# Performance work log

Hardware: AMD Instinct MI355X
Metric: run time of the kernel (lower is better)

The kernel has to match this reference:

```python
import jax, jax.numpy as jnp
import numpy as np

D = 1024   # hidden_size
H = 16     # n_head
K = 64     # head_size
B = 4
T = 1024
LAYER_ID = 12
NUM_LAYERS = 24
D_MIX = 32
D_DECAY = 64


def setup_inputs() -> dict:
    key = jax.random.key(0)
    ks = jax.random.split(key, 12)
    r01 = LAYER_ID / (NUM_LAYERS - 1)          # ratio_0_to_1
    r10 = 1.0 - LAYER_ID / NUM_LAYERS          # ratio_1_to_almost0
    ddd = jnp.arange(D, dtype=jnp.float32) / D
    maa = lambda p: (1.0 - ddd ** p).reshape(1, 1, D)
    inp = {}
    inp['x'] = jax.random.normal(ks[0], (B, T, D), jnp.float32)
    inp['time_maa_x'] = maa(r10)
    inp['time_maa_w'] = maa(r10)
    inp['time_maa_k'] = maa(r10)
    inp['time_maa_v'] = (1.0 - (ddd ** r10 + 0.3 * r01)).reshape(1, 1, D)
    inp['time_maa_r'] = maa(0.5 * r10)
    inp['time_maa_g'] = maa(0.5 * r10)
    # torch inits time_maa_w1 to zeros (trivial); use small uniform like w2 for a non-degenerate test
    inp['time_maa_w1'] = jax.random.uniform(ks[1], (D, D_MIX * 5), jnp.float32, -0.01, 0.01)
    inp['time_maa_w2'] = jax.random.uniform(ks[2], (5, D_MIX, D), jnp.float32, -0.01, 0.01)
    n = jnp.arange(D, dtype=jnp.float32)
    inp['time_decay'] = (-6.0 + 5.0 * (n / (D - 1)) ** (0.7 + 1.3 * r01)).reshape(1, 1, D)
    inp['time_decay_w1'] = jax.random.uniform(ks[3], (D, D_DECAY), jnp.float32, -0.01, 0.01)
    inp['time_decay_w2'] = jax.random.uniform(ks[4], (D_DECAY, D), jnp.float32, -0.01, 0.01)
    for nm, kk in zip(['W_r', 'W_k', 'W_v', 'W_g', 'W_o'], ks[5:10]):
        inp[nm] = jax.random.normal(kk, (D, D), jnp.float32) * 0.02
    inp['ln_w'] = jnp.ones((D,), jnp.float32)
    inp['ln_b'] = jnp.zeros((D,), jnp.float32)
    return inp


def _bidir_shift(x):
    # (x[i-1] + x[i+1]) / 2 with zero padding at the boundaries
    left = jnp.pad(x[:, :-1, :], ((0, 0), (1, 0), (0, 0)))
    right = jnp.pad(x[:, 1:, :], ((0, 0), (0, 1), (0, 0)))
    return 0.5 * (left + right)


def _lion_attention(r, k, v, w):
    # r,k,v,w: (B,H,T,Khd), w = -exp(decay) <= 0
    Tn = r.shape[2]
    cs = jnp.cumsum(w, axis=2)
    cs_b = cs - w
    shift_f = cs[:, :, Tn // 2:Tn // 2 + 1, :]
    shift_b = cs_b[:, :, Tn // 2:Tn // 2 + 1, :]
    cf = jnp.clip(cs - shift_f, -60.0, 60.0)
    cb = jnp.clip(cs_b - shift_b, -60.0, 60.0)
    # A_fwd = tril(Q*e^{cf} @ (K*e^{-cf})^T); A_bwd = triu(Q*e^{-cb} @ (K*e^{cb})^T, 1)
    A_f = jnp.einsum('bhik,bhjk->bhij', r * jnp.exp(cf), k * jnp.exp(-cf))
    A_b = jnp.einsum('bhik,bhjk->bhij', r * jnp.exp(-cb), k * jnp.exp(cb))
    idx = jnp.arange(Tn)
    lower = idx[:, None] >= idx[None, :]   # tril incl. diagonal
    A = jnp.where(lower, A_f, A_b)         # == tril(A_f) + triu(A_b, 1)
    return jnp.einsum('bhij,bhjk->bhik', A, v)


def reference(x, time_maa_x, time_maa_w, time_maa_k, time_maa_v, time_maa_r, time_maa_g,
              time_maa_w1, time_maa_w2, time_decay, time_decay_w1, time_decay_w2,
              W_r, W_k, W_v, W_g, W_o, ln_w, ln_b):
    Bn, Tn, Dn = x.shape
    Hh, Kk = H, Dn // H
    dxprev = _bidir_shift(x) - x
    # data-dependent token-shift mixing coefficients (LoRA-style)
    xxx = jnp.tanh((x + dxprev * time_maa_x) @ time_maa_w1)          # (B,T,5*32)
    mm = jnp.einsum('btfm,fmd->fbtd', xxx.reshape(Bn, Tn, 5, D_MIX), time_maa_w2)
    mw, mk, mv, mr, mg = mm[0], mm[1], mm[2], mm[3], mm[4]
    xw = x + dxprev * (time_maa_w + mw)
    xk = x + dxprev * (time_maa_k + mk)
    xv = x + dxprev * (time_maa_v + mv)
    xr = x + dxprev * (time_maa_r + mr)
    xg = x + dxprev * (time_maa_g + mg)
    r = xr @ W_r.T
    k = xk @ W_k.T
    v = xv @ W_v.T
    g = jax.nn.silu(xg @ W_g.T)
    w = time_decay + jnp.tanh(xw @ time_decay_w1) @ time_decay_w2   # (B,T,D)
    to_h = lambda t: t.reshape(Bn, Tn, Hh, Kk).transpose(0, 2, 1, 3)
    y = _lion_attention(to_h(r), to_h(k), to_h(v), -jnp.exp(to_h(w)))
    y = y.transpose(0, 2, 1, 3).reshape(Bn * Tn, Dn)
    # GroupNorm(n_head groups, eps = 1e-5 * head_size_divisor^2)
    eps = 1e-5 * 64.0
    yg = y.reshape(Bn * Tn, Hh, Kk)
    mu = jnp.mean(yg, axis=-1, keepdims=True)
    var = jnp.var(yg, axis=-1, keepdims=True)
    yn = ((yg - mu) * jax.lax.rsqrt(var + eps)).reshape(Bn * Tn, Dn) * ln_w + ln_b
    y = yn.reshape(Bn, Tn, Dn)
    return (y * g) @ W_o.T
```

## Files before the change

kernel.cpp:

```cpp
#include <hip/hip_runtime.h>
#include <math.h>

#define NB 4
#define TT 1024
#define DD 1024
#define NTOK 4096
#define ND (NTOK*DD)

typedef __attribute__((ext_vector_type(8))) short bh8;
typedef __attribute__((ext_vector_type(4))) float fx4;

__device__ __forceinline__ unsigned short f2bf(float f) {
    unsigned int b = __float_as_uint(f);
    b += 0x7fffu + ((b >> 16) & 1u);
    return (unsigned short)(b >> 16);
}

__device__ __forceinline__ unsigned pkbf(float a, float b) {
#if __has_builtin(__builtin_amdgcn_cvt_pk_bf16_f32)
    auto r = __builtin_amdgcn_cvt_pk_bf16_f32(a, b);
    unsigned u;
    __builtin_memcpy(&u, &r, 4);
    return u;
#else
    return ((unsigned)f2bf(b) << 16) | f2bf(a);
#endif
}

#define GLD16(gp, lp) __builtin_amdgcn_global_load_lds( \
    (__attribute__((address_space(1))) void*)(gp), \
    (__attribute__((address_space(3))) void*)(lp), 16, 0, 0)

#define BARF() do { __builtin_amdgcn_s_barrier(); asm volatile("" ::: "memory"); } while (0)

__global__ __launch_bounds__(256) void k_prep(const float* __restrict__ W_r, const float* __restrict__ W_k,
                                              const float* __restrict__ W_v, const float* __restrict__ W_g,
                                              const float* __restrict__ W_o,
                                              const float* __restrict__ w1, const float* __restrict__ dw1,
                                              const float* __restrict__ w2,
                                              unsigned short* __restrict__ Wrb, unsigned short* __restrict__ Wkb,
                                              unsigned short* __restrict__ Wvb, unsigned short* __restrict__ Wgb,
                                              unsigned short* __restrict__ Wob,
                                              unsigned short* __restrict__ w1T, unsigned short* __restrict__ dw1T,
                                              unsigned short* __restrict__ w2T16) {
    int y = blockIdx.y, bx = blockIdx.x, tid = threadIdx.x;
    if (y < 5) {
        if (bx >= 512) return;
        const float* s = (y == 0) ? W_r : (y == 1) ? W_k : (y == 2) ? W_v : (y == 3) ? W_g : W_o;
        unsigned short* d = (y == 0) ? Wrb : (y == 1) ? Wkb : (y == 2) ? Wvb : (y == 3) ? Wgb : Wob;
        int i = (bx * 256 + tid) * 8;
        float4 a = *(const float4*)(s + i);
        float4 b = *(const float4*)(s + i + 4);
        uint4 o;
        o.x = pkbf(a.x, a.y);
        o.y = pkbf(a.z, a.w);
        o.z = pkbf(b.x, b.y);
        o.w = pkbf(b.z, b.w);
        *(uint4*)(d + i) = o;
    } else if (y == 5) {
        int o = bx * 256 + tid;
        int r = o & 1023, c = o >> 10;
        w1T[o] = f2bf(w1[r * 160 + c]);
    } else {
        if (bx < 256) {
            int o = bx * 256 + tid;
            int r = o & 1023, c = o >> 10;
            dw1T[o] = f2bf(dw1[r * 64 + c]);
        } else if (bx < 276) {
            int wi = bx - 256;
            int f = wi >> 2;
            int d = (wi & 3) * 256 + tid;
#pragma unroll 8
            for (int m = 0; m < 32; m++)
                w2T16[(size_t)(f * 1024 + d) * 32 + m] = f2bf(w2[(size_t)(f * 32 + m) * 1024 + d]);
        }
    }
}

__global__ __launch_bounds__(256) void k_mixx(const float* __restrict__ x,
                                              const float* __restrict__ maa_x,
                                              unsigned short* __restrict__ xmix16) {
    int base = (blockIdx.x * 256 + threadIdx.x) * 4;
    int t = (base >> 10) & 1023;
    int d = base & 1023;
    float4 xv = *(const float4*)(x + base);
    float4 xm = (t > 0)    ? *(const float4*)(x + base - 1024) : make_float4(0, 0, 0, 0);
    float4 xp = (t < 1023) ? *(const float4*)(x + base + 1024) : make_float4(0, 0, 0, 0);
    float4 ma = *(const float4*)(maa_x + d);
    uint2 o;
    float a0 = xv.x + (0.5f * (xm.x + xp.x) - xv.x) * ma.x;
    float a1 = xv.y + (0.5f * (xm.y + xp.y) - xv.y) * ma.y;
    float a2 = xv.z + (0.5f * (xm.z + xp.z) - xv.z) * ma.z;
    float a3 = xv.w + (0.5f * (xm.w + xp.w) - xv.w) * ma.w;
    o.x = pkbf(a0, a1);
    o.y = pkbf(a2, a3);
    *(uint2*)(xmix16 + base) = o;
}

__global__ __launch_bounds__(64) void k_xxx2(const unsigned short* __restrict__ xmix16,
                                             const unsigned short* __restrict__ w1T,
                                             unsigned short* __restrict__ xxx16) {
    int lane = threadIdx.x;
    int l15 = lane & 15, qd = lane >> 4;
    int m0 = blockIdx.x * 16;
    fx4 acc[10];
#pragma unroll
    for (int nt = 0; nt < 10; nt++)
#pragma unroll
        for (int r = 0; r < 4; r++) acc[nt][r] = 0.f;
#pragma unroll 2
    for (int kb = 0; kb < 1024; kb += 32) {
        bh8 af = *(const bh8*)(xmix16 + (size_t)(m0 + l15) * 1024 + kb + qd * 8);
#pragma unroll
        for (int nt = 0; nt < 10; nt++) {
            bh8 bf = *(const bh8*)(w1T + (size_t)(nt * 16 + l15) * 1024 + kb + qd * 8);
            acc[nt] = __builtin_amdgcn_mfma_f32_16x16x32_bf16(af, bf, acc[nt], 0, 0, 0);
        }
    }
#pragma unroll
    for (int nt = 0; nt < 10; nt++)
#pragma unroll
        for (int r = 0; r < 4; r++)
            xxx16[(size_t)(m0 + qd * 4 + r) * 160 + nt * 16 + l15] = f2bf(tanhf(acc[nt][r]));
}

__global__ __launch_bounds__(256, 2) void k_mmix(const float* __restrict__ x,
                                                 const unsigned short* __restrict__ xxx16,
                                                 const unsigned short* __restrict__ w2T16,
                                                 const float* __restrict__ maa_w,
                                                 const float* __restrict__ maa_k,
                                                 const float* __restrict__ maa_v,
                                                 const float* __restrict__ maa_r,
                                                 const float* __restrict__ maa_g,
                                                 unsigned short* __restrict__ xw16,
                                                 unsigned short* __restrict__ xk16,
                                                 unsigned short* __restrict__ xv16,
                                                 unsigned short* __restrict__ xr16,
                                                 unsigned short* __restrict__ xg16) {
    int tid = threadIdx.x;
    int w = tid >> 6, lane = tid & 63, l15 = lane & 15, qd = lane >> 4;
    int n0 = blockIdx.x * 64;
    int m0w = blockIdx.y * 128 + w * 32;
    const float* maap[5] = {maa_w, maa_k, maa_v, maa_r, maa_g};
    unsigned short* outp[5] = {xw16, xk16, xv16, xr16, xg16};
    float xin[8][4], dxv[8][4];
#pragma unroll
    for (int mi = 0; mi < 2; mi++)
#pragma unroll
        for (int r = 0; r < 4; r++) {
            int tok = m0w + mi * 16 + qd * 4 + r;
            int t = tok & 1023;
#pragma unroll
            for (int ni = 0; ni < 4; ni++) {
                int d = n0 + ni * 16 + l15;
                size_t idx = (size_t)tok * 1024 + d;
                float xv = x[idx];
                float xm1 = (t > 0)    ? x[idx - 1024] : 0.f;
                float xp1 = (t < 1023) ? x[idx + 1024] : 0.f;
                xin[mi * 4 + r][ni] = xv;
                dxv[mi * 4 + r][ni] = 0.5f * (xm1 + xp1) - xv;
            }
        }
#pragma unroll
    for (int f = 0; f < 5; f++) {
        bh8 af[2], bf[4];
#pragma unroll
        for (int mi = 0; mi < 2; mi++)
            af[mi] = *(const bh8*)(xxx16 + (size_t)(m0w + mi * 16 + l15) * 160 + f * 32 + qd * 8);
#pragma unroll
        for (int ni = 0; ni < 4; ni++)
            bf[ni] = *(const bh8*)(w2T16 + (size_t)(f * 1024 + n0 + ni * 16 + l15) * 32 + qd * 8);
        fx4 acc[2][4];
#pragma unroll
        for (int mi = 0; mi < 2; mi++)
#pragma unroll
            for (int ni = 0; ni < 4; ni++) {
#pragma unroll
                for (int r = 0; r < 4; r++) acc[mi][ni][r] = 0.f;
                acc[mi][ni] = __builtin_amdgcn_mfma_f32_16x16x32_bf16(af[mi], bf[ni], acc[mi][ni], 0, 0, 0);
            }
        const float* maa = maap[f];
        unsigned short* op = outp[f];
#pragma unroll
        for (int ni = 0; ni < 4; ni++) {
            float mv = maa[n0 + ni * 16 + l15];
#pragma unroll
            for (int mi = 0; mi < 2; mi++)
#pragma unroll
                for (int r = 0; r < 4; r++) {
                    float o = xin[mi * 4 + r][ni] + dxv[mi * 4 + r][ni] * (mv + acc[mi][ni][r]);
                    op[(size_t)(m0w + mi * 16 + qd * 4 + r) * 1024 + n0 + ni * 16 + l15] = f2bf(o);
                }
        }
    }
}

__global__ __launch_bounds__(64) void k_dec1m(const unsigned short* __restrict__ xw16,
                                              const unsigned short* __restrict__ dw1T,
                                              float* __restrict__ dech) {
    int lane = threadIdx.x;
    int l15 = lane & 15, qd = lane >> 4;
    int m0 = blockIdx.x * 16;
    fx4 acc[4];
#pragma unroll
    for (int nt = 0; nt < 4; nt++)
#pragma unroll
        for (int r = 0; r < 4; r++) acc[nt][r] = 0.f;
#pragma unroll 2
    for (int kb = 0; kb < 1024; kb += 32) {
        bh8 af = *(const bh8*)(xw16 + (size_t)(m0 + l15) * 1024 + kb + qd * 8);
#pragma unroll
        for (int nt = 0; nt < 4; nt++) {
            bh8 bf = *(const bh8*)(dw1T + (size_t)(nt * 16 + l15) * 1024 + kb + qd * 8);
            acc[nt] = __builtin_amdgcn_mfma_f32_16x16x32_bf16(af, bf, acc[nt], 0, 0, 0);
        }
    }
#pragma unroll
    for (int nt = 0; nt < 4; nt++)
#pragma unroll
        for (int r = 0; r < 4; r++)
            dech[(size_t)(m0 + qd * 4 + r) * 64 + nt * 16 + l15] = tanhf(acc[nt][r]);
}

__global__ __launch_bounds__(256) void k_dec2(const float* __restrict__ dech,
                                              const float* __restrict__ dw2,
                                              const float* __restrict__ tdec,
                                              float* __restrict__ ew) {
    __shared__ float hl[8][64];
    int tid = threadIdx.x;
    int tok0 = blockIdx.x * 8;
    {
        int l = tid;        hl[l >> 6][l & 63] = dech[tok0 * 64 + l];
        l = tid + 256;      hl[l >> 6][l & 63] = dech[tok0 * 64 + l];
    }
    __syncthreads();
#pragma unroll 1
    for (int c = 0; c < 4; c++) {
        int d = c * 256 + tid;
        float acc[8] = {};
#pragma unroll 8
        for (int j = 0; j < 64; j++) {
            float wv = dw2[j * 1024 + d];
#pragma unroll
            for (int g = 0; g < 8; g++) acc[g] = fmaf(hl[g][j], wv, acc[g]);
        }
        float td = tdec[d];
#pragma unroll
        for (int g = 0; g < 8; g++) ew[(tok0 + g) * 1024 + d] = -expf(td + acc[g]);
    }
}

__global__ __launch_bounds__(64) void k_scan1(const float* __restrict__ ew, float* __restrict__ segsum) {
    int bx = blockIdx.x;
    int b = bx >> 9, seg = (bx >> 4) & 31, dch = bx & 15;
    int d = dch * 64 + threadIdx.x;
    size_t base = ((size_t)(b * 1024 + seg * 32)) * 1024 + d;
    float s = 0.f;
#pragma unroll 8
    for (int t = 0; t < 32; t++) s += ew[base + (size_t)t * 1024];
    segsum[(b * 32 + seg) * 1024 + d] = s;
}

__global__ __launch_bounds__(64) void k_scan3(const float* __restrict__ ew, const float* __restrict__ segsum,
                                              float* __restrict__ cf, float* __restrict__ cb) {
    int bx = blockIdx.x;
    int b = bx >> 9, seg = (bx >> 4) & 31, dch = bx & 15;
    int d = dch * 64 + threadIdx.x;
    float run = 0.f, pre = 0.f, off16 = 0.f;
#pragma unroll
    for (int s = 0; s < 32; s++) {
        float tv = segsum[(b * 32 + s) * 1024 + d];
        if (s == seg) pre = run;
        if (s == 16) off16 = run;
        run += tv;
    }
    float e512 = ew[((size_t)(b * 1024 + 512)) * 1024 + d];
    float sb = off16;
    float sf = off16 + e512;
    float cum = pre;
    size_t base = ((size_t)(b * 1024 + seg * 32)) * 1024 + d;
#pragma unroll 4
    for (int t = 0; t < 32; t++) {
        float prev = cum;
        cum += ew[base + (size_t)t * 1024];
        cf[base + (size_t)t * 1024] = fminf(fmaxf(cum - sf, -60.f), 60.f);
        cb[base + (size_t)t * 1024] = fminf(fmaxf(prev - sb, -60.f), 60.f);
    }
}

#define QST(slotoff, kbv) do { \
    unsigned short* _sa = (unsigned short*)(smem + (slotoff)); \
    unsigned short* _sb = _sa + 8192; \
    GLD16(aSrc + (size_t)(kbv),             _sa + (w * 64) * 32); \
    GLD16(aSrc + (size_t)(kbv) + 16 * 1024, _sa + (w * 64 + 16) * 32); \
    GLD16(aSrc + (size_t)(kbv) + 32 * 1024, _sa + (w * 64 + 32) * 32); \
    GLD16(aSrc + (size_t)(kbv) + 48 * 1024, _sa + (w * 64 + 48) * 32); \
    GLD16(bSrc + (size_t)(kbv),             _sb + (w * 32) * 32); \
    GLD16(bSrc + (size_t)(kbv) + 16 * 1024, _sb + (w * 32 + 16) * 32); \
} while (0)

__device__ __forceinline__ void gemm_v4(const unsigned short* __restrict__ A,
                                        const unsigned short* __restrict__ W,
                                        int m0, int n0, int mode,
                                        float* __restrict__ Cf,
                                        unsigned short* __restrict__ O1,
                                        unsigned short* __restrict__ O2,
                                        const float* __restrict__ cfp,
                                        const float* __restrict__ cbp,
                                        char* smem) {
    int tid = threadIdx.x;
    int lane = tid & 63, w = tid >> 6;
    int l15 = lane & 15, qd = lane >> 4;
    int wm = w >> 1, wn = w & 1;
    int lr = lane >> 2, lb = lane & 3;
    int gblk = lb ^ ((lr >> 1) & 3);
    const unsigned short* aSrc = A + (size_t)(m0 + w * 64 + lr) * 1024 + gblk * 8;
    const unsigned short* bSrc = W + (size_t)(n0 + w * 32 + lr) * 1024 + gblk * 8;
    int rc = (qd ^ ((l15 >> 1) & 3)) * 8;
    int arow = (wm * 128 + l15) * 32 + rc;
    int brow = (wn * 64 + l15) * 32 + rc;

    fx4 acc[8][4];
#pragma unroll
    for (int mt = 0; mt < 8; mt++)
#pragma unroll
        for (int nt = 0; nt < 4; nt++)
#pragma unroll
            for (int r = 0; r < 4; r++) acc[mt][nt][r] = 0.f;

    QST(0, 0);
    QST(24576, 32);
    asm volatile("s_waitcnt vmcnt(6)" ::: "memory");
    BARF();

    int oc = 0, on = 24576, o2 = 49152;
#pragma unroll 1
    for (int t = 0; t < 32; ++t) {
        if (t < 30) QST(o2, (t + 2) * 32);
        const unsigned short* cA = (const unsigned short*)(smem + oc);
        const unsigned short* cB = cA + 8192;
        bh8 a[8], b[4];
#pragma unroll
        for (int mt = 0; mt < 8; ++mt) a[mt] = *(const bh8*)(cA + arow + mt * 512);
#pragma unroll
        for (int nt = 0; nt < 4; ++nt) b[nt] = *(const bh8*)(cB + brow + nt * 512);
        __builtin_amdgcn_s_setprio(1);
#pragma unroll
        for (int nt = 0; nt < 4; ++nt)
#pragma unroll
            for (int mt = 0; mt < 8; ++mt)
                acc[mt][nt] = __builtin_amdgcn_mfma_f32_16x16x32_bf16(a[mt], b[nt], acc[mt][nt], 0, 0, 0);
        __builtin_amdgcn_s_setprio(0);
        asm volatile("s_waitcnt lgkmcnt(0)" ::: "memory");
        if (t < 30)       asm volatile("s_waitcnt vmcnt(6)" ::: "memory");
        else if (t == 30) asm volatile("s_waitcnt vmcnt(0)" ::: "memory");
        BARF();
        int tmp = oc; oc = on; on = o2; o2 = tmp;
    }

    int mbase = m0 + wm * 128;
    int nb = n0 + wn * 64;
    if (mode <= 1) {
#pragma unroll
        for (int mt = 0; mt < 8; mt++)
#pragma unroll
            for (int nt = 0; nt < 4; nt++)
#pragma unroll
                for (int r = 0; r < 4; r++) {
                    float v = acc[mt][nt][r];
                    if (mode == 1) v = v / (1.f + __expf(-v));
                    Cf[(size_t)(mbase + mt * 16 + qd * 4 + r) * 1024 + nb + nt * 16 + l15] = v;
                }
    } else if (mode <= 3) {
        float s1 = (mode == 2) ? 1.f : -1.f;
#pragma unroll
        for (int mt = 0; mt < 8; mt++)
#pragma unroll
            for (int nt = 0; nt < 4; nt++)
#pragma unroll
                for (int r = 0; r < 4; r++) {
                    size_t idx = (size_t)(mbase + mt * 16 + qd * 4 + r) * 1024 + nb + nt * 16 + l15;
                    float v = acc[mt][nt][r];
                    O1[idx] = f2bf(v * __expf(s1 * cfp[idx]));
                    O2[idx] = f2bf(v * __expf(-s1 * cbp[idx]));
                }
    } else {
        unsigned short* T = (unsigned short*)smem;
        int bq = m0 >> 10, t0 = m0 & 1023;
#pragma unroll
        for (int mt = 0; mt < 8; mt++)
#pragma unroll
            for (int nt = 0; nt < 4; nt++) {
                int dl = wn * 64 + nt * 16 + l15;
                int tl = wm * 128 + mt * 16 + qd * 4;
                uint2 pk2;
                pk2.x = pkbf(acc[mt][nt][0], acc[mt][nt][1]);
                pk2.y = pkbf(acc[mt][nt][2], acc[mt][nt][3]);
                *(uint2*)(T + dl * 268 + tl) = pk2;
            }
        asm volatile("s_waitcnt lgkmcnt(0)" ::: "memory");
        BARF();
#pragma unroll
        for (int i = 0; i < 16; ++i) {
            int idx = i * 256 + tid;
            int dd = idx >> 5, u = idx & 31;
            uint4 vv = *(const uint4*)(T + dd * 268 + u * 8);
            *(uint4*)(O1 + (size_t)(bq * 1024 + n0 + dd) * 1024 + t0 + u * 8) = vv;
        }
    }
}

__global__ __launch_bounds__(256, 2) void k_qkvg(const unsigned short* __restrict__ xr16,
                                                 const unsigned short* __restrict__ xk16,
                                                 const unsigned short* __restrict__ xv16,
                                                 const unsigned short* __restrict__ xg16,
                                                 const unsigned short* __restrict__ Wrb,
                                                 const unsigned short* __restrict__ Wkb,
                                                 const unsigned short* __restrict__ Wvb,
                                                 const unsigned short* __restrict__ Wgb,
                                                 unsigned short* __restrict__ qf, unsigned short* __restrict__ qb,
                                                 unsigned short* __restrict__ kf, unsigned short* __restrict__ kb,
                                                 unsigned short* __restrict__ vvt,
                                                 float* __restrict__ gg,
                                                 const float* __restrict__ cf, const float* __restrict__ cb) {
    __shared__ __align__(16) char smem[73728];
    int flat = blockIdx.x;
    int wkid = (flat & 7) * 64 + (flat >> 3);
    int gy = wkid >> 7;
    int rem = wkid & 127;
    int m0 = (rem >> 3) * 256, n0 = (rem & 7) * 128;
    const unsigned short* Ap = (gy == 0) ? xr16 : (gy == 1) ? xk16 : (gy == 2) ? xv16 : xg16;
    const unsigned short* Wp = (gy == 0) ? Wrb : (gy == 1) ? Wkb : (gy == 2) ? Wvb : Wgb;
    int mode = (gy == 0) ? 2 : (gy == 1) ? 3 : (gy == 2) ? 4 : 1;
    unsigned short* o1 = (gy == 0) ? qf : (gy == 1) ? kf : (gy == 2) ? vvt : nullptr;
    unsigned short* o2 = (gy == 0) ? qb : (gy == 1) ? kb : nullptr;
    float* cfo = (gy == 3) ? gg : nullptr;
    gemm_v4(Ap, Wp, m0, n0, mode, cfo, o1, o2, cf, cb, smem);
}

__global__ __launch_bounds__(256, 2) void k_gemmo(const unsigned short* __restrict__ z16,
                                                  const unsigned short* __restrict__ Wob,
                                                  float* __restrict__ out) {
    __shared__ __align__(16) char smem[73728];
    int flat = blockIdx.x;
    int wkid = (flat & 7) * 16 + (flat >> 3);
    int m0 = (wkid >> 3) * 256, n0 = (wkid & 7) * 128;
    gemm_v4(z16, Wob, m0, n0, 0, out, nullptr, nullptr, nullptr, nullptr, smem);
}

__global__ __launch_bounds__(256, 2) void k_attn(const unsigned short* __restrict__ qf,
                                                 const unsigned short* __restrict__ qb,
                                                 const unsigned short* __restrict__ kf,
                                                 const unsigned short* __restrict__ kb,
                                                 const unsigned short* __restrict__ vvt,
                                                 float* __restrict__ y) {
    __shared__ __align__(16) char smem[16384];
    unsigned short* sK = (unsigned short*)smem;
    unsigned short* sV = (unsigned short*)(smem + 8192);
    int tid = threadIdx.x;
    int w = tid >> 6, lane = tid & 63, l15 = lane & 15, qd = lane >> 4;
    int bid = blockIdx.x;
    int bh = (bid & 7) + ((bid >> 6) << 3);
    int ib = (bid >> 3) & 7;
    int b = bh >> 4, h = bh & 15;
    int i0w = ib * 128 + w * 32;
    int bt0 = b * 1024;
    const unsigned short* vrow = vvt + (size_t)(b * 1024 + h * 64 + w * 16 + l15) * 1024 + qd * 8;
    int fmax = (i0w + 31) >> 6;
    int bmin = i0w >> 6;
    int srcA = l15 + ((lane & 16) << 1);
    int srcB = srcA + 16;
    fx4 yacc[4][2];
#pragma unroll
    for (int mt = 0; mt < 4; mt++)
#pragma unroll
        for (int nt = 0; nt < 2; nt++)
#pragma unroll
            for (int r = 0; r < 4; r++) yacc[mt][nt][r] = 0.f;

    for (int phase = 0; phase < 2; phase++) {
        const unsigned short* Q = phase ? qb : qf;
        const unsigned short* K = phase ? kb : kf;
        bh8 qfr[2][2];
#pragma unroll
        for (int nt = 0; nt < 2; nt++)
#pragma unroll
            for (int ks = 0; ks < 2; ks++)
                qfr[nt][ks] = *(const bh8*)(Q + (size_t)(bt0 + i0w + nt * 16 + l15) * 1024
                                              + h * 64 + ks * 32 + qd * 8);
        int jlo = phase == 0 ? 0 : 2 * ib;
        int jhi = phase == 0 ? 2 * ib + 1 : 15;
        const unsigned short* krow = K + (size_t)(bt0 + w * 16 + l15) * 1024 + h * 64 + qd * 8;
        for (int jt = jlo; jt <= jhi; jt++) {
            int jb = jt * 64;
            __syncthreads();
            GLD16(krow + (size_t)jb * 1024,        sK + w * 512);
            GLD16(krow + (size_t)jb * 1024 + 32,   sK + 2048 + w * 512);
            GLD16(vrow + jb,                        sV + w * 512);
            GLD16(vrow + jb + 32,                   sV + 2048 + w * 512);
            __syncthreads();
            bool active = (phase == 0) ? (jt <= fmax) : (jt >= bmin);
            if (!active) continue;
            bool needmask = (phase == 0) ? (jb + 63 > i0w) : (i0w + 31 >= jb);
            bh8 kc[8];
#pragma unroll
            for (int fi = 0; fi < 8; fi++)
                kc[fi] = *(const bh8*)(sK + fi * 512 + lane * 8);
            fx4 sacc[4][2];
#pragma unroll
            for (int mt = 0; mt < 4; mt++)
#pragma unroll
                for (int nt = 0; nt < 2; nt++)
#pragma unroll
                    for (int r = 0; r < 4; r++) sacc[mt][nt][r] = 0.f;
#pragma unroll
            for (int ks = 0; ks < 2; ks++)
#pragma unroll
                for (int mt = 0; mt < 4; mt++)
#pragma unroll
                    for (int nt = 0; nt < 2; nt++)
                        sacc[mt][nt] = __builtin_amdgcn_mfma_f32_16x16x32_bf16(kc[ks * 4 + mt], qfr[nt][ks], sacc[mt][nt], 0, 0, 0);
            uint2 pk[4][2];
#pragma unroll
            for (int mt = 0; mt < 4; mt++)
#pragma unroll
                for (int nt = 0; nt < 2; nt++) {
                    fx4 s = sacc[mt][nt];
                    if (needmask) {
                        int ii = i0w + nt * 16 + l15;
                        int jj0 = jb + mt * 16 + qd * 4;
#pragma unroll
                        for (int r = 0; r < 4; r++) {
                            bool keep = (phase == 0) ? (ii >= jj0 + r) : (ii < jj0 + r);
                            if (!keep) s[r] = 0.f;
                        }
                    }
                    pk[mt][nt].x = pkbf(s[0], s[1]);
                    pk[mt][nt].y = pkbf(s[2], s[3]);
                }
            bh8 vc[8];
#pragma unroll
            for (int fi = 0; fi < 8; fi++)
                vc[fi] = *(const bh8*)(sV + fi * 512 + lane * 8);
#pragma unroll
            for (int ks2 = 0; ks2 < 2; ks2++) {
#pragma unroll
                for (int nt = 0; nt < 2; nt++) {
                    int lox  = __shfl((int)pk[2 * ks2][nt].x,     srcA);
                    int hix  = __shfl((int)pk[2 * ks2 + 1][nt].x, srcA);
                    int loy  = __shfl((int)pk[2 * ks2][nt].y,     srcA);
                    int hiy  = __shfl((int)pk[2 * ks2 + 1][nt].y, srcA);
                    int lox2 = __shfl((int)pk[2 * ks2][nt].x,     srcB);
                    int hix2 = __shfl((int)pk[2 * ks2 + 1][nt].x, srcB);
                    int loy2 = __shfl((int)pk[2 * ks2][nt].y,     srcB);
                    int hiy2 = __shfl((int)pk[2 * ks2 + 1][nt].y, srcB);
                    union { int4 i; bh8 h; } cv;
                    cv.i.x = (qd & 2) ? hix  : lox;
                    cv.i.y = (qd & 2) ? hiy  : loy;
                    cv.i.z = (qd & 2) ? hix2 : lox2;
                    cv.i.w = (qd & 2) ? hiy2 : loy2;
#pragma unroll
                    for (int mt = 0; mt < 4; mt++)
                        yacc[mt][nt] = __builtin_amdgcn_mfma_f32_16x16x32_bf16(vc[ks2 * 4 + mt], cv.h, yacc[mt][nt], 0, 0, 0);
                }
            }
        }
    }
#pragma unroll
    for (int mt = 0; mt < 4; mt++)
#pragma unroll
        for (int nt = 0; nt < 2; nt++) {
            fx4 s = yacc[mt][nt];
            float4 o; o.x = s[0]; o.y = s[1]; o.z = s[2]; o.w = s[3];
            *(float4*)&y[(size_t)(bt0 + i0w + nt * 16 + l15) * 1024 + h * 64 + mt * 16 + qd * 4] = o;
        }
}

__global__ __launch_bounds__(256) void k_gn(const float* __restrict__ y,
                                            const float* __restrict__ g,
                                            const float* __restrict__ lnw,
                                            const float* __restrict__ lnb,
                                            unsigned short* __restrict__ z16) {
    int tid = threadIdx.x;
    int lane = tid & 63;
    int wv = tid >> 6;
    int group = blockIdx.x * 4 + wv;
    int tok = group >> 4, h = group & 15;
    int d = h * 64 + lane;
    size_t idx = (size_t)tok * 1024 + d;
    float val = y[idx];
    float s = val, s2 = val * val;
#pragma unroll
    for (int off = 32; off > 0; off >>= 1) {
        s  += __shfl_xor(s, off, 64);
        s2 += __shfl_xor(s2, off, 64);
    }
    float mu = s * (1.f / 64.f);
    float var = s2 * (1.f / 64.f) - mu * mu;
    float inv = rsqrtf(var + 6.4e-4f);
    float yn = (val - mu) * inv * lnw[d] + lnb[d];
    z16[idx] = f2bf(yn * g[idx]);
}

extern "C" void kernel_launch(void* const* d_in, const int* in_sizes, int n_in,
                              void* d_out, int out_size, void* d_ws, size_t ws_size,
                              hipStream_t stream) {
    const float* x     = (const float*)d_in[0];
    const float* maa_x = (const float*)d_in[1];
    const float* maa_w = (const float*)d_in[2];
    const float* maa_k = (const float*)d_in[3];
    const float* maa_v = (const float*)d_in[4];
    const float* maa_r = (const float*)d_in[5];
    const float* maa_g = (const float*)d_in[6];
    const float* w1    = (const float*)d_in[7];
    const float* w2    = (const float*)d_in[8];
    const float* tdec  = (const float*)d_in[9];
    const float* dw1   = (const float*)d_in[10];
    const float* dw2   = (const float*)d_in[11];
    const float* W_r   = (const float*)d_in[12];
    const float* W_k   = (const float*)d_in[13];
    const float* W_v   = (const float*)d_in[14];
    const float* W_g   = (const float*)d_in[15];
    const float* W_o   = (const float*)d_in[16];
    const float* lnw   = (const float*)d_in[17];
    const float* lnb   = (const float*)d_in[18];

    float* ws = (float*)d_ws;
    size_t o = 0;
    float* dech   = ws + o; o += 262144;
    float* segsum = ws + o; o += 131072;
    float* ew     = ws + o; o += 4194304;
    float* cf     = ws + o; o += 4194304;
    float* cb     = ws + o; o += 4194304;
    float* gg     = ws + o; o += 4194304;
    unsigned short* us = (unsigned short*)(ws + o);
    size_t u = 0;
    unsigned short* xmix16 = us + u; u += 4194304;
    unsigned short* xw16 = us + u; u += 4194304;
    unsigned short* xr16 = us + u; u += 4194304;
    unsigned short* xk16 = us + u; u += 4194304;
    unsigned short* xv16 = us + u; u += 4194304;
    unsigned short* xg16 = us + u; u += 4194304;
    unsigned short* qf   = us + u; u += 4194304;
    unsigned short* qb   = us + u; u += 4194304;
    unsigned short* kf   = us + u; u += 4194304;
    unsigned short* kb   = us + u; u += 4194304;
    unsigned short* vvt  = us + u; u += 4194304;
    unsigned short* Wrb  = us + u; u += 1048576;
    unsigned short* Wkb  = us + u; u += 1048576;
    unsigned short* Wvb  = us + u; u += 1048576;
    unsigned short* Wgb  = us + u; u += 1048576;
    unsigned short* Wob  = us + u; u += 1048576;
    unsigned short* w1T  = us + u; u += 163840;
    unsigned short* dw1T = us + u; u += 65536;
    unsigned short* xxx16 = us + u; u += 655360;
    unsigned short* w2T16 = us + u; u += 163840;
    float* yb0 = cf;
    unsigned short* z16 = xr16;

    k_prep<<<dim3(640, 7), 256, 0, stream>>>(W_r, W_k, W_v, W_g, W_o, w1, dw1, w2,
                                             Wrb, Wkb, Wvb, Wgb, Wob, w1T, dw1T, w2T16);
    k_mixx<<<4096, 256, 0, stream>>>(x, maa_x, xmix16);
    k_xxx2<<<256, 64, 0, stream>>>(xmix16, w1T, xxx16);
    k_mmix<<<dim3(16, 32), 256, 0, stream>>>(x, xxx16, w2T16, maa_w, maa_k, maa_v, maa_r, maa_g,
                                             xw16, xk16, xv16, xr16, xg16);
    k_dec1m<<<256, 64, 0, stream>>>(xw16, dw1T, dech);
    k_dec2<<<512, 256, 0, stream>>>(dech, dw2, tdec, ew);
    k_scan1<<<2048, 64, 0, stream>>>(ew, segsum);
    k_scan3<<<2048, 64, 0, stream>>>(ew, segsum, cf, cb);
    k_qkvg<<<dim3(512), dim3(256), 0, stream>>>(xr16, xk16, xv16, xg16, Wrb, Wkb, Wvb, Wgb,
                                                qf, qb, kf, kb, vvt, gg, cf, cb);
    k_attn<<<512, 256, 0, stream>>>(qf, qb, kf, kb, vvt, yb0);
    k_gn<<<16384, 256, 0, stream>>>(yb0, gg, lnw, lnb, z16);
    k_gemmo<<<128, 256, 0, stream>>>(z16, Wob, (float*)d_out);
}
```

Measured before the change: 340.6 us.

## Retile GEMMs with templated warp layout and batch two KV tiles per attention sync

Turns the shared GEMM routine into a template over warp count and N tile width. The QKVG projection now runs 8 waves on 128x256 tiles, and the output projection runs 4 waves on 128x128 tiles with twice as many blocks, so each wave holds a smaller 64x64 accumulator and occupancy can rise. The attention kernel loads two K/V tiles per synchronisation pair into a doubled shared buffer to halve barrier count. The cost is more shared memory in attention, and possibly wasted loads of inactive tiles at the odd-length range end.

```diff
diff --git a/kernel.cpp b/kernel.cpp
--- a/kernel.cpp
+++ b/kernel.cpp
@@ -288,18 +288,8 @@
     }
 }
 
-#define QST(slotoff, kbv) do { \
-    unsigned short* _sa = (unsigned short*)(smem + (slotoff)); \
-    unsigned short* _sb = _sa + 8192; \
-    GLD16(aSrc + (size_t)(kbv),             _sa + (w * 64) * 32); \
-    GLD16(aSrc + (size_t)(kbv) + 16 * 1024, _sa + (w * 64 + 16) * 32); \
-    GLD16(aSrc + (size_t)(kbv) + 32 * 1024, _sa + (w * 64 + 32) * 32); \
-    GLD16(aSrc + (size_t)(kbv) + 48 * 1024, _sa + (w * 64 + 48) * 32); \
-    GLD16(bSrc + (size_t)(kbv),             _sb + (w * 32) * 32); \
-    GLD16(bSrc + (size_t)(kbv) + 16 * 1024, _sb + (w * 32 + 16) * 32); \
-} while (0)
-
-__device__ __forceinline__ void gemm_v4(const unsigned short* __restrict__ A,
+template<int NW, int BNv>
+__device__ __forceinline__ void gemm_v5(const unsigned short* __restrict__ A,
                                         const unsigned short* __restrict__ W,
                                         int m0, int n0, int mode,
                                         float* __restrict__ Cf,
@@ -308,78 +298,101 @@
                                         const float* __restrict__ cfp,
                                         const float* __restrict__ cbp,
                                         char* smem) {
+    constexpr int AR = 128 / NW;
+    constexpr int AG = AR / 16;
+    constexpr int BR = BNv / NW;
+    constexpr int BG = BR / 16;
+    constexpr int LPW = AG + BG;
+    constexpr int SLOT = (128 + BNv) * 64;
+    constexpr int WNC = BNv / 64;
+
     int tid = threadIdx.x;
     int lane = tid & 63, w = tid >> 6;
     int l15 = lane & 15, qd = lane >> 4;
-    int wm = w >> 1, wn = w & 1;
+    int wm = w / WNC, wn = w % WNC;
     int lr = lane >> 2, lb = lane & 3;
     int gblk = lb ^ ((lr >> 1) & 3);
-    const unsigned short* aSrc = A + (size_t)(m0 + w * 64 + lr) * 1024 + gblk * 8;
-    const unsigned short* bSrc = W + (size_t)(n0 + w * 32 + lr) * 1024 + gblk * 8;
+    const unsigned short* aSrc = A + (size_t)(m0 + w * AR + lr) * 1024 + gblk * 8;
+    const unsigned short* bSrc = W + (size_t)(n0 + w * BR + lr) * 1024 + gblk * 8;
     int rc = (qd ^ ((l15 >> 1) & 3)) * 8;
-    int arow = (wm * 128 + l15) * 32 + rc;
+    int arow = (wm * 64 + l15) * 32 + rc;
     int brow = (wn * 64 + l15) * 32 + rc;
 
-    fx4 acc[8][4];
-#pragma unroll
-    for (int mt = 0; mt < 8; mt++)
+    auto stage = [&](int off, int kbv) {
+        unsigned short* _sa = (unsigned short*)(smem + off);
+        unsigned short* _sb = _sa + 128 * 32;
+#pragma unroll
+        for (int i = 0; i < AG; ++i)
+            GLD16(aSrc + kbv + (size_t)i * 16 * 1024, _sa + (w * AR + i * 16) * 32);
+#pragma unroll
+        for (int i = 0; i < BG; ++i)
+            GLD16(bSrc + kbv + (size_t)i * 16 * 1024, _sb + (w * BR + i * 16) * 32);
+    };
+
+    fx4 acc[4][4];
+#pragma unroll
+    for (int mt = 0; mt < 4; mt++)
 #pragma unroll
         for (int nt = 0; nt < 4; nt++)
 #pragma unroll
             for (int r = 0; r < 4; r++) acc[mt][nt][r] = 0.f;
 
-    QST(0, 0);
-    QST(24576, 32);
-    asm volatile("s_waitcnt vmcnt(6)" ::: "memory");
+    stage(0, 0);
+    stage(SLOT, 32);
+    if constexpr (LPW == 3) asm volatile("s_waitcnt vmcnt(3)" ::: "memory");
+    else                    asm volatile("s_waitcnt vmcnt(4)" ::: "memory");
     BARF();
 
-    int oc = 0, on = 24576, o2 = 49152;
+    int oc = 0, on = SLOT, o2 = 2 * SLOT;
 #pragma unroll 1
     for (int t = 0; t < 32; ++t) {
-        if (t < 30) QST(o2, (t + 2) * 32);
+        if (t < 30) stage(o2, (t + 2) * 32);
         const unsigned short* cA = (const unsigned short*)(smem + oc);
-        const unsigned short* cB = cA + 8192;
-        bh8 a[8], b[4];
-#pragma unroll
-        for (int mt = 0; mt < 8; ++mt) a[mt] = *(const bh8*)(cA + arow + mt * 512);
+        const unsigned short* cB = cA + 128 * 32;
+        bh8 a[4], b[4];
+#pragma unroll
+        for (int mt = 0; mt < 4; ++mt) a[mt] = *(const bh8*)(cA + arow + mt * 512);
 #pragma unroll
         for (int nt = 0; nt < 4; ++nt) b[nt] = *(const bh8*)(cB + brow + nt * 512);
         __builtin_amdgcn_s_setprio(1);
 #pragma unroll
         for (int nt = 0; nt < 4; ++nt)
 #pragma unroll
-            for (int mt = 0; mt < 8; ++mt)
+            for (int mt = 0; mt < 4; ++mt)
                 acc[mt][nt] = __builtin_amdgcn_mfma_f32_16x16x32_bf16(a[mt], b[nt], acc[mt][nt], 0, 0, 0);
         __builtin_amdgcn_s_setprio(0);
         asm volatile("s_waitcnt lgkmcnt(0)" ::: "memory");
-        if (t < 30)       asm volatile("s_waitcnt vmcnt(6)" ::: "memory");
-        else if (t == 30) asm volatile("s_waitcnt vmcnt(0)" ::: "memory");
+        if (t < 30) {
+            if constexpr (LPW == 3) asm volatile("s_waitcnt vmcnt(3)" ::: "memory");
+            else                    asm volatile("s_waitcnt vmcnt(4)" ::: "memory");
+        } else if (t == 30) {
+            asm volatile("s_waitcnt vmcnt(0)" ::: "memory");
+        }
         BARF();
         int tmp = oc; oc = on; on = o2; o2 = tmp;
     }
 
-    int mbase = m0 + wm * 128;
-    int nb = n0 + wn * 64;
+    int mb = m0 + wm * 64, nb = n0 + wn * 64;
     if (mode <= 1) {
 #pragma unroll
-        for (int mt = 0; mt < 8; mt++)
+        for (int mt = 0; mt < 4; mt++)
 #pragma unroll
             for (int nt = 0; nt < 4; nt++)
 #pragma unroll
                 for (int r = 0; r < 4; r++) {
                     float v = acc[mt][nt][r];
                     if (mode == 1) v = v / (1.f + __expf(-v));
-                    Cf[(size_t)(mbase + mt * 16 + qd * 4 + r) * 1024 + nb + nt * 16 + l15] = v;
+                    Cf[(size_t)(mb + mt * 16 + qd * 4 + r) * 1024 + nb + nt * 16 + l15] = v;
                 }
     } else if (mode <= 3) {
         float s1 = (mode == 2) ? 1.f : -1.f;
 #pragma unroll
-        for (int mt = 0; mt < 8; mt++)
+        for (int mt = 0; mt < 4; mt++)
 #pragma unroll
             for (int nt = 0; nt < 4; nt++)
 #pragma unroll
                 for (int r = 0; r < 4; r++) {
-                    size_t idx = (size_t)(mbase + mt * 16 + qd * 4 + r) * 1024 + nb + nt * 16 + l15;
+                    size_t idx = (size_t)(mb + mt * 16 + qd * 4 + r) * 1024 + nb + nt * 16 + l15;
                     float v = acc[mt][nt][r];
                     O1[idx] = f2bf(v * __expf(s1 * cfp[idx]));
                     O2[idx] = f2bf(v * __expf(-s1 * cbp[idx]));
@@ -388,29 +401,29 @@
         unsigned short* T = (unsigned short*)smem;
         int bq = m0 >> 10, t0 = m0 & 1023;
 #pragma unroll
-        for (int mt = 0; mt < 8; mt++)
+        for (int mt = 0; mt < 4; mt++)
 #pragma unroll
             for (int nt = 0; nt < 4; nt++) {
                 int dl = wn * 64 + nt * 16 + l15;
-                int tl = wm * 128 + mt * 16 + qd * 4;
+                int tl = wm * 64 + mt * 16 + qd * 4;
                 uint2 pk2;
                 pk2.x = pkbf(acc[mt][nt][0], acc[mt][nt][1]);
                 pk2.y = pkbf(acc[mt][nt][2], acc[mt][nt][3]);
-                *(uint2*)(T + dl * 268 + tl) = pk2;
+                *(uint2*)(T + dl * 136 + tl) = pk2;
             }
         asm volatile("s_waitcnt lgkmcnt(0)" ::: "memory");
         BARF();
 #pragma unroll
-        for (int i = 0; i < 16; ++i) {
-            int idx = i * 256 + tid;
-            int dd = idx >> 5, u = idx & 31;
-            uint4 vv = *(const uint4*)(T + dd * 268 + u * 8);
+        for (int p = 0; p < 8; ++p) {
+            int idx = p * (NW * 64) + tid;
+            int dd = idx >> 4, u = idx & 15;
+            uint4 vv = *(const uint4*)(T + dd * 136 + u * 8);
             *(uint4*)(O1 + (size_t)(bq * 1024 + n0 + dd) * 1024 + t0 + u * 8) = vv;
         }
     }
 }
 
-__global__ __launch_bounds__(256, 2) void k_qkvg(const unsigned short* __restrict__ xr16,
+__global__ __launch_bounds__(512, 4) void k_qkvg(const unsigned short* __restrict__ xr16,
                                                  const unsigned short* __restrict__ xk16,
                                                  const unsigned short* __restrict__ xv16,
                                                  const unsigned short* __restrict__ xg16,
@@ -428,24 +441,24 @@
     int wkid = (flat & 7) * 64 + (flat >> 3);
     int gy = wkid >> 7;
     int rem = wkid & 127;
-    int m0 = (rem >> 3) * 256, n0 = (rem & 7) * 128;
+    int m0 = (rem >> 2) * 128, n0 = (rem & 3) * 256;
     const unsigned short* Ap = (gy == 0) ? xr16 : (gy == 1) ? xk16 : (gy == 2) ? xv16 : xg16;
     const unsigned short* Wp = (gy == 0) ? Wrb : (gy == 1) ? Wkb : (gy == 2) ? Wvb : Wgb;
     int mode = (gy == 0) ? 2 : (gy == 1) ? 3 : (gy == 2) ? 4 : 1;
     unsigned short* o1 = (gy == 0) ? qf : (gy == 1) ? kf : (gy == 2) ? vvt : nullptr;
     unsigned short* o2 = (gy == 0) ? qb : (gy == 1) ? kb : nullptr;
     float* cfo = (gy == 3) ? gg : nullptr;
-    gemm_v4(Ap, Wp, m0, n0, mode, cfo, o1, o2, cf, cb, smem);
-}
-
-__global__ __launch_bounds__(256, 2) void k_gemmo(const unsigned short* __restrict__ z16,
+    gemm_v5<8, 256>(Ap, Wp, m0, n0, mode, cfo, o1, o2, cf, cb, smem);
+}
+
+__global__ __launch_bounds__(256, 3) void k_gemmo(const unsigned short* __restrict__ z16,
                                                   const unsigned short* __restrict__ Wob,
                                                   float* __restrict__ out) {
-    __shared__ __align__(16) char smem[73728];
+    __shared__ __align__(16) char smem[49152];
     int flat = blockIdx.x;
-    int wkid = (flat & 7) * 16 + (flat >> 3);
-    int m0 = (wkid >> 3) * 256, n0 = (wkid & 7) * 128;
-    gemm_v4(z16, Wob, m0, n0, 0, out, nullptr, nullptr, nullptr, nullptr, smem);
+    int wkid = (flat & 7) * 32 + (flat >> 3);
+    int m0 = (wkid >> 3) * 128, n0 = (wkid & 7) * 128;
+    gemm_v5<4, 128>(z16, Wob, m0, n0, 0, out, nullptr, nullptr, nullptr, nullptr, smem);
 }
 
 __global__ __launch_bounds__(256, 2) void k_attn(const unsigned short* __restrict__ qf,
@@ -454,9 +467,9 @@
                                                  const unsigned short* __restrict__ kb,
                                                  const unsigned short* __restrict__ vvt,
                                                  float* __restrict__ y) {
-    __shared__ __align__(16) char smem[16384];
+    __shared__ __align__(16) char smem[32768];
     unsigned short* sK = (unsigned short*)smem;
-    unsigned short* sV = (unsigned short*)(smem + 8192);
+    unsigned short* sV = (unsigned short*)(smem + 16384);
     int tid = threadIdx.x;
     int w = tid >> 6, lane = tid & 63, l15 = lane & 15, qd = lane >> 4;
     int bid = blockIdx.x;
@@ -491,77 +504,87 @@
         int jlo = phase == 0 ? 0 : 2 * ib;
         int jhi = phase == 0 ? 2 * ib + 1 : 15;
         const unsigned short* krow = K + (size_t)(bt0 + w * 16 + l15) * 1024 + h * 64 + qd * 8;
-        for (int jt = jlo; jt <= jhi; jt++) {
-            int jb = jt * 64;
+        for (int jt2 = jlo; jt2 <= jhi; jt2 += 2) {
             __syncthreads();
-            GLD16(krow + (size_t)jb * 1024,        sK + w * 512);
-            GLD16(krow + (size_t)jb * 1024 + 32,   sK + 2048 + w * 512);
-            GLD16(vrow + jb,                        sV + w * 512);
-            GLD16(vrow + jb + 32,                   sV + 2048 + w * 512);
+#pragma unroll
+            for (int u = 0; u < 2; ++u) {
+                size_t jb = (size_t)(jt2 + u) * 64;
+                GLD16(krow + jb * 1024,        sK + u * 4096 + w * 512);
+                GLD16(krow + jb * 1024 + 32,   sK + u * 4096 + 2048 + w * 512);
+                GLD16(vrow + jb,               sV + u * 4096 + w * 512);
+                GLD16(vrow + jb + 32,          sV + u * 4096 + 2048 + w * 512);
+            }
             __syncthreads();
-            bool active = (phase == 0) ? (jt <= fmax) : (jt >= bmin);
-            if (!active) continue;
-            bool needmask = (phase == 0) ? (jb + 63 > i0w) : (i0w + 31 >= jb);
-            bh8 kc[8];
-#pragma unroll
-            for (int fi = 0; fi < 8; fi++)
-                kc[fi] = *(const bh8*)(sK + fi * 512 + lane * 8);
-            fx4 sacc[4][2];
-#pragma unroll
-            for (int mt = 0; mt < 4; mt++)
-#pragma unroll
-                for (int nt = 0; nt < 2; nt++)
-#pragma unroll
-                    for (int r = 0; r < 4; r++) sacc[mt][nt][r] = 0.f;
-#pragma unroll
-            for (int ks = 0; ks < 2; ks++)
+#pragma unroll
+            for (int u = 0; u < 2; ++u) {
+                int jt = jt2 + u;
+                int jb = jt * 64;
+                const unsigned short* bK = sK + u * 4096;
+                const unsigned short* bV = sV + u * 4096;
+                bool active = (phase == 0) ? (jt <= fmax) : (jt >= bmin);
+                if (!active) continue;
+                bool needmask = (phase == 0) ? (jb + 63 > i0w) : (i0w + 31 >= jb);
+                bh8 kc[8];
+#pragma unroll
+                for (int fi = 0; fi < 8; fi++)
+                    kc[fi] = *(const bh8*)(bK + fi * 512 + lane * 8);
+                fx4 sacc[4][2];
 #pragma unroll
                 for (int mt = 0; mt < 4; mt++)
 #pragma unroll
                     for (int nt = 0; nt < 2; nt++)
-                        sacc[mt][nt] = __builtin_amdgcn_mfma_f32_16x16x32_bf16(kc[ks * 4 + mt], qfr[nt][ks], sacc[mt][nt], 0, 0, 0);
-            uint2 pk[4][2];
-#pragma unroll
-            for (int mt = 0; mt < 4; mt++)
-#pragma unroll
-                for (int nt = 0; nt < 2; nt++) {
-                    fx4 s = sacc[mt][nt];
-                    if (needmask) {
-                        int ii = i0w + nt * 16 + l15;
-                        int jj0 = jb + mt * 16 + qd * 4;
-#pragma unroll
-                        for (int r = 0; r < 4; r++) {
-                            bool keep = (phase == 0) ? (ii >= jj0 + r) : (ii < jj0 + r);
-                            if (!keep) s[r] = 0.f;
+#pragma unroll
+                        for (int r = 0; r < 4; r++) sacc[mt][nt][r] = 0.f;
+#pragma unroll
+                for (int ks = 0; ks < 2; ks++)
+#pragma unroll
+                    for (int mt = 0; mt < 4; mt++)
+#pragma unroll
+                        for (int nt = 0; nt < 2; nt++)
+                            sacc[mt][nt] = __builtin_amdgcn_mfma_f32_16x16x32_bf16(kc[ks * 4 + mt], qfr[nt][ks], sacc[mt][nt], 0, 0, 0);
+                uint2 pk[4][2];
+#pragma unroll
+                for (int mt = 0; mt < 4; mt++)
+#pragma unroll
+                    for (int nt = 0; nt < 2; nt++) {
+                        fx4 s = sacc[mt][nt];
+                        if (needmask) {
+                            int ii = i0w + nt * 16 + l15;
+                            int jj0 = jb + mt * 16 + qd * 4;
+#pragma unroll
+                            for (int r = 0; r < 4; r++) {
+                                bool keep = (phase == 0) ? (ii >= jj0 + r) : (ii < jj0 + r);
+                                if (!keep) s[r] = 0.f;
+                            }
                         }
+                        pk[mt][nt].x = pkbf(s[0], s[1]);
+                        pk[mt][nt].y = pkbf(s[2], s[3]);
                     }
-                    pk[mt][nt].x = pkbf(s[0], s[1]);
-                    pk[mt][nt].y = pkbf(s[2], s[3]);
-                }
-            bh8 vc[8];
-#pragma unroll
-            for (int fi = 0; fi < 8; fi++)
-                vc[fi] = *(const bh8*)(sV + fi * 512 + lane * 8);
-#pragma unroll
-            for (int ks2 = 0; ks2 < 2; ks2++) {
-#pragma unroll
-                for (int nt = 0; nt < 2; nt++) {
-                    int lox  = __shfl((int)pk[2 * ks2][nt].x,     srcA);
-                    int hix  = __shfl((int)pk[2 * ks2 + 1][nt].x, srcA);
-                    int loy  = __shfl((int)pk[2 * ks2][nt].y,     srcA);
-                    int hiy  = __shfl((int)pk[2 * ks2 + 1][nt].y, srcA);
-                    int lox2 = __shfl((int)pk[2 * ks2][nt].x,     srcB);
-                    int hix2 = __shfl((int)pk[2 * ks2 + 1][nt].x, srcB);
-                    int loy2 = __shfl((int)pk[2 * ks2][nt].y,     srcB);
-                    int hiy2 = __shfl((int)pk[2 * ks2 + 1][nt].y, srcB);
-                    union { int4 i; bh8 h; } cv;
-                    cv.i.x = (qd & 2) ? hix  : lox;
-                    cv.i.y = (qd & 2) ? hiy  : loy;
-                    cv.i.z = (qd & 2) ? hix2 : lox2;
-                    cv.i.w = (qd & 2) ? hiy2 : loy2;
-#pragma unroll
-                    for (int mt = 0; mt < 4; mt++)
-                        yacc[mt][nt] = __builtin_amdgcn_mfma_f32_16x16x32_bf16(vc[ks2 * 4 + mt], cv.h, yacc[mt][nt], 0, 0, 0);
+                bh8 vc[8];
+#pragma unroll
+                for (int fi = 0; fi < 8; fi++)
+                    vc[fi] = *(const bh8*)(bV + fi * 512 + lane * 8);
+#pragma unroll
+                for (int ks2 = 0; ks2 < 2; ks2++) {
+#pragma unroll
+                    for (int nt = 0; nt < 2; nt++) {
+                        int lox  = __shfl((int)pk[2 * ks2][nt].x,     srcA);
+                        int hix  = __shfl((int)pk[2 * ks2 + 1][nt].x, srcA);
+                        int loy  = __shfl((int)pk[2 * ks2][nt].y,     srcA);
+                        int hiy  = __shfl((int)pk[2 * ks2 + 1][nt].y, srcA);
+                        int lox2 = __shfl((int)pk[2 * ks2][nt].x,     srcB);
+                        int hix2 = __shfl((int)pk[2 * ks2 + 1][nt].x, srcB);
+                        int loy2 = __shfl((int)pk[2 * ks2][nt].y,     srcB);
+                        int hiy2 = __shfl((int)pk[2 * ks2 + 1][nt].y, srcB);
+                        union { int4 i; bh8 h; } cv;
+                        cv.i.x = (qd & 2) ? hix  : lox;
+                        cv.i.y = (qd & 2) ? hiy  : loy;
+                        cv.i.z = (qd & 2) ? hix2 : lox2;
+                        cv.i.w = (qd & 2) ? hiy2 : loy2;
+#pragma unroll
+                        for (int mt = 0; mt < 4; mt++)
+                            yacc[mt][nt] = __builtin_amdgcn_mfma_f32_16x16x32_bf16(vc[ks2 * 4 + mt], cv.h, yacc[mt][nt], 0, 0, 0);
+                    }
                 }
             }
         }
@@ -668,9 +691,9 @@
     k_dec2<<<512, 256, 0, stream>>>(dech, dw2, tdec, ew);
     k_scan1<<<2048, 64, 0, stream>>>(ew, segsum);
     k_scan3<<<2048, 64, 0, stream>>>(ew, segsum, cf, cb);
-    k_qkvg<<<dim3(512), dim3(256), 0, stream>>>(xr16, xk16, xv16, xg16, Wrb, Wkb, Wvb, Wgb,
+    k_qkvg<<<dim3(512), dim3(512), 0, stream>>>(xr16, xk16, xv16, xg16, Wrb, Wkb, Wvb, Wgb,
                                                 qf, qb, kf, kb, vvt, gg, cf, cb);
     k_attn<<<512, 256, 0, stream>>>(qf, qb, kf, kb, vvt, yb0);
     k_gn<<<16384, 256, 0, stream>>>(yb0, gg, lnw, lnb, z16);
-    k_gemmo<<<128, 256, 0, stream>>>(z16, Wob, (float*)d_out);
-}
+    k_gemmo<<<256, 256, 0, stream>>>(z16, Wob, (float*)d_out);
+}
```

Result: faster. 321.6 us (-5.6%).
